# Optimization experiments

Hardware: AMD Instinct MI355X
Metric: run time of the kernel (lower is better)

The kernel has to match this reference:

```python
import jax, jax.numpy as jnp
import numpy as np

B_, L_, DM, DS, DC, EX = 4, 2048, 1024, 16, 4, 2
DI = DM * EX

def setup_inputs() -> dict:
    key = jax.random.key(0)
    ks = jax.random.split(key, 8)
    s = lambda i, shape, scale: jax.random.normal(ks[i], shape, jnp.float32) * scale
    return dict(
        x=s(0, (B_, L_, DM), 1.0),
        in_proj_w=s(1, (2 * DI, DM), 0.02),
        conv_weight=s(2, (DI, DC), 0.1),
        conv_bias=jnp.zeros((DI,), jnp.float32),
        A_log=jax.random.uniform(ks[3], (DS,), jnp.float32, -4.0, -1.0),
        D=jnp.ones((DI,), jnp.float32),
        delta_w=s(4, (DS, DI), 0.02),
        delta_b=jnp.ones((DS,), jnp.float32),
        B_w=s(5, (DS, DI), 0.02),
        C_w=s(6, (DS, DI), 0.02),
        out_proj_w=s(7, (DM, DI), 0.02),
    )

def reference(x, in_proj_w, conv_weight, conv_bias, A_log, D, delta_w, delta_b, B_w, C_w, out_proj_w):
    Bb, L, Dm = x.shape
    di, dc = conv_weight.shape
    # 1. input projection and split into ssm / gate branches
    x_inner = x @ in_proj_w.T                       # [B,L,2*di]
    x_ssm, x_gate = x_inner[..., :di], x_inner[..., di:]
    # 2. causal depthwise conv1d + SiLU (kernel size dc, per-channel weights)
    xp = jnp.pad(x_ssm, ((0, 0), (dc - 1, 0), (0, 0)))
    xc = conv_bias + sum(xp[:, k:k + L, :] * conv_weight[:, k] for k in range(dc))
    x_conv = jax.nn.silu(xc)                         # [B,L,di]
    # 3. content-aware discretization
    delta = jax.nn.softplus(x_conv @ delta_w.T + delta_b)  # [B,L,N]
    Bs = x_conv @ B_w.T                              # [B,L,N]
    Cs = x_conv @ C_w.T                              # [B,L,N]
    A = -jnp.exp(A_log)                              # [N]
    xavg = x_conv.mean(axis=-1)                      # [B,L]
    # 4. selective SSM scan over L with state h:[B,N]
    def step(h, inp):
        dt, bt, ct, xa = inp                         # [B,N],[B,N],[B,N],[B]
        h = jnp.exp(dt * A) * h + dt * bt * xa[:, None]
        return h, (h * ct).sum(-1)                   # y_t: [B]
    h0 = jnp.zeros((Bb, A.shape[0]), x.dtype)
    _, ys = jax.lax.scan(
        step, h0,
        (delta.transpose(1, 0, 2), Bs.transpose(1, 0, 2), Cs.transpose(1, 0, 2), xavg.T))
    y_ssm = ys.T[..., None]                          # [B,L,1] (broadcasts over di)
    # 5. gate, skip, output projection
    y_gated = y_ssm * jax.nn.silu(x_gate)
    y_skip = y_gated + x_conv * D
    return y_skip @ out_proj_w.T                     # [B,L,D]
```

## Files before the change

kernel.cpp:

```cpp
#include <hip/hip_runtime.h>
#include <cmath>

#define LL 2048
#define NROW 8192
#define DMODEL 1024
#define DINNER 2048
#define NSTATE 16
#define NSEG 64
#define SEGLEN 32

typedef unsigned short u16;
typedef __attribute__((ext_vector_type(8))) unsigned short u16x8;
typedef __attribute__((ext_vector_type(8))) short short8;
typedef __attribute__((ext_vector_type(4))) float floatx4;
typedef __attribute__((ext_vector_type(16))) float floatx16;

__device__ __forceinline__ float bf2f(u16 h) {
    unsigned u = ((unsigned)h) << 16;
    float f;
    __builtin_memcpy(&f, &u, 4);
    return f;
}
__device__ __forceinline__ u16 f2bf(float f) {
    unsigned u;
    __builtin_memcpy(&u, &f, 4);
    u = u + 0x7fffu + ((u >> 16) & 1u);
    return (u16)(u >> 16);
}
__device__ __forceinline__ float silu_f(float x) { return x / (1.f + __expf(-x)); }

__global__ __launch_bounds__(256) void cvt_multi(
    const float* __restrict__ s0, const float* __restrict__ s1,
    const float* __restrict__ s2, const float* __restrict__ s3,
    const float* __restrict__ s4, const float* __restrict__ s5,
    u16* __restrict__ d0, u16* __restrict__ d1, u16* __restrict__ d2,
    u16* __restrict__ d3, u16* __restrict__ d4, u16* __restrict__ d5) {
    int bid = blockIdx.x;
    const float* s;
    u16* d;
    size_t off;
    if (bid < 4096)      { s = s0; d = d0; off = (size_t)bid * 2048; }
    else if (bid < 6144) { s = s1; d = d1; off = (size_t)(bid - 4096) * 2048; }
    else if (bid < 7168) { s = s2; d = d2; off = (size_t)(bid - 6144) * 2048; }
    else if (bid < 7184) { s = s3; d = d3; off = (size_t)(bid - 7168) * 2048; }
    else if (bid < 7200) { s = s4; d = d4; off = (size_t)(bid - 7184) * 2048; }
    else                 { s = s5; d = d5; off = (size_t)(bid - 7200) * 2048; }
    size_t i = off + (size_t)threadIdx.x * 8;
    float4 a = *(const float4*)&s[i];
    float4 b = *(const float4*)&s[i + 4];
    u16x8 o;
    o[0] = f2bf(a.x); o[1] = f2bf(a.y); o[2] = f2bf(a.z); o[3] = f2bf(a.w);
    o[4] = f2bf(b.x); o[5] = f2bf(b.y); o[6] = f2bf(b.z); o[7] = f2bf(b.w);
    *(u16x8*)&d[i] = o;
}

#define GL_LDS(gp, lp)                                                        \
    __builtin_amdgcn_global_load_lds(                                         \
        (const __attribute__((address_space(1))) void*)(gp),                  \
        (__attribute__((address_space(3))) void*)(lp), 16, 0, 0)
#define BAR() __builtin_amdgcn_s_barrier()
#define SB0() __builtin_amdgcn_sched_barrier(0)
#define LGKM0()                                                               \
    do {                                                                      \
        asm volatile("s_waitcnt lgkmcnt(0)" ::: "memory");                    \
        __builtin_amdgcn_sched_barrier(0);                                    \
    } while (0)
#define VMC4() asm volatile("s_waitcnt vmcnt(4)" ::: "memory")
#define VMC2() asm volatile("s_waitcnt vmcnt(2)" ::: "memory")
#define PRIO1() __builtin_amdgcn_s_setprio(1)
#define PRIO0() __builtin_amdgcn_s_setprio(0)

template <int OUT_BF16>
__global__ __launch_bounds__(512, 2) void gemm_bt_256(
    const u16* __restrict__ A, const u16* __restrict__ B,
    void* __restrict__ Cout, int N, int K) {
    __shared__ u16 sAf[2 * 2 * 128 * 64];
    __shared__ u16 sBf[2 * 2 * 128 * 64];
    const int tid = threadIdx.x;
    const int lane = tid & 63;
    const int wave = tid >> 6;
    const int wm = wave >> 2;
    const int wn = wave & 3;

    const int gx = gridDim.x;
    const int nwg = gx * gridDim.y;
    const int cpx = nwg >> 3;
    int lin = blockIdx.y * gx + blockIdx.x;
    int swz = (lin & 7) * cpx + (lin >> 3);
    const int bm = (swz / gx) * 256;
    const int bn = (swz % gx) * 256;

    const int gslot = (lane & 7) ^ ((lane >> 3) & 7);
    const int srowoff = lane >> 3;
    const u16* aStage = A + (size_t)(bm + wave * 8 + srowoff) * K + gslot * 8 + 64;
    const u16* bStage = B + (size_t)(bn + wave * 8 + srowoff) * K + gslot * 8 + 128;
    const size_t row64 = (size_t)64 * K;
    const size_t row128 = (size_t)128 * K;

#define STAGE_A(BUF, H, PTR)                                                  \
    do {                                                                      \
        GL_LDS((PTR) + (H) * row128,         &sAf[(BUF) * 16384 + (H) * 8192 + wave * 512]); \
        GL_LDS((PTR) + (H) * row128 + row64, &sAf[(BUF) * 16384 + (H) * 8192 + (8 + wave) * 512]); \
    } while (0)
#define STAGE_B(BUF, H, PTR)                                                  \
    do {                                                                      \
        GL_LDS((PTR) + (H) * row128,         &sBf[(BUF) * 16384 + (H) * 8192 + wave * 512]); \
        GL_LDS((PTR) + (H) * row128 + row64, &sBf[(BUF) * 16384 + (H) * 8192 + (8 + wave) * 512]); \
    } while (0)

    const int fr = lane & 15;
    const int kq = lane >> 4;
    const int st0 = kq ^ (fr & 7);
    const int st1 = (4 + kq) ^ (fr & 7);
    const int aRd0 = wm * 8192 + fr * 64 + st0 * 8;
    const int aRd1 = wm * 8192 + fr * 64 + st1 * 8;
    const int bRow = (wn & 1) * 64 + fr;
    const int bRd0 = (wn >> 1) * 8192 + bRow * 64 + st0 * 8;
    const int bRd1 = (wn >> 1) * 8192 + bRow * 64 + st1 * 8;

#define RD_A(dst, BUF, R0)                                                    \
    do {                                                                      \
        _Pragma("unroll")                                                     \
        for (int mi = 0; mi < 4; ++mi) {                                      \
            dst[mi][0] = *(const short8*)&sAf[(BUF) * 16384 + aRd0 + ((R0) + mi * 16) * 64]; \
            dst[mi][1] = *(const short8*)&sAf[(BUF) * 16384 + aRd1 + ((R0) + mi * 16) * 64]; \
        }                                                                     \
    } while (0)
#define RD_B(dst, BUF, R0)                                                    \
    do {                                                                      \
        _Pragma("unroll")                                                     \
        for (int ni = 0; ni < 2; ++ni) {                                      \
            dst[ni][0] = *(const short8*)&sBf[(BUF) * 16384 + bRd0 + ((R0) + ni * 16) * 64]; \
            dst[ni][1] = *(const short8*)&sBf[(BUF) * 16384 + bRd1 + ((R0) + ni * 16) * 64]; \
        }                                                                     \
    } while (0)
#define MFMA_PH(AF, RB, BF, CB)                                               \
    do {                                                                      \
        _Pragma("unroll")                                                     \
        for (int kh = 0; kh < 2; ++kh)                                        \
            _Pragma("unroll")                                                 \
            for (int mi = 0; mi < 4; ++mi)                                    \
                _Pragma("unroll")                                             \
                for (int ni = 0; ni < 2; ++ni)                                \
                    acc[(RB) + mi][(CB) + ni] =                               \
                        __builtin_amdgcn_mfma_f32_16x16x32_bf16(              \
                            AF[mi][kh], BF[ni][kh],                           \
                            acc[(RB) + mi][(CB) + ni], 0, 0, 0);              \
    } while (0)

    floatx4 acc[8][4];
#pragma unroll
    for (int i = 0; i < 8; ++i)
#pragma unroll
        for (int j = 0; j < 4; ++j) acc[i][j] = (floatx4){0.f, 0.f, 0.f, 0.f};

    short8 afX[4][2], afY[4][2], bf01[2][2], bf23[2][2];

    {
        const u16* a0 = aStage - 64;
        const u16* b0 = bStage - 128;
        STAGE_A(0, 0, a0);
        STAGE_A(0, 1, a0);
        STAGE_B(0, 0, b0);
        STAGE_B(0, 1, b0);
        STAGE_B(1, 0, b0 + 64);
        STAGE_B(1, 1, b0 + 64);
    }
    VMC4();
    BAR();
    RD_A(afX, 0, 0);
    RD_B(bf01, 0, 0);
    SB0();

#define TILE(CUR, NXT)                                                        \
                      \
    LGKM0();                                                                  \
    PRIO1();                                                                  \
    MFMA_PH(afX, 0, bf01, 0);                                                 \
    PRIO0();                                                                  \
    SB0();                                                                    \
    RD_B(bf23, CUR, 32);                                                      \
    STAGE_A(NXT, 0, aStage);                                                  \
    SB0();                                                                    \
             \
    LGKM0();                                                                  \
    PRIO1();                                                                  \
    MFMA_PH(afX, 0, bf23, 2);                                                 \
    PRIO0();                                                                  \
    SB0();                                                                    \
    RD_A(afY, CUR, 64);                                                       \
    STAGE_A(NXT, 1, aStage);                                                  \
    VMC4();                                                \
    BAR();                                                                    \
                     \
    LGKM0();                                                                  \
    PRIO1();                                                                  \
    MFMA_PH(afY, 4, bf01, 0);                                                 \
    PRIO0();                                                                  \
    SB0();                                                                    \
    RD_B(bf01, NXT, 0);                                                       \
    STAGE_B(CUR, 0, bStage);                                                  \
    SB0();                                                                    \
            \
    PRIO1();                                                                  \
    MFMA_PH(afY, 4, bf23, 2);                                                 \
    PRIO0();                                                                  \
    SB0();                                                                    \
    STAGE_B(CUR, 1, bStage);                                                  \
    VMC4();                                                \
    BAR();                                                                    \
    RD_A(afX, NXT, 0);                                                        \
    SB0();                                                                    \
    aStage += 64;                                                             \
    bStage += 64;

    const int NT = K >> 6;
    for (int t = 0; t < NT; t += 2) {
        TILE(0, 1)
        TILE(1, 0)
    }
#undef TILE

    const int cc = lane & 15;
    const int rb = (lane >> 4) * 4;
#pragma unroll
    for (int mi = 0; mi < 8; ++mi)
#pragma unroll
        for (int ni = 0; ni < 4; ++ni)
#pragma unroll
            for (int r = 0; r < 4; ++r) {
                int grow = bm + wm * 128 + mi * 16 + rb + r;
                int gcol = bn + wn * 64 + ni * 16 + cc;
                float v = acc[mi][ni][r];
                if (OUT_BF16)
                    ((u16*)Cout)[(size_t)grow * N + gcol] = f2bf(v);
                else
                    ((float*)Cout)[(size_t)grow * N + gcol] = v;
            }
#undef STAGE_A
#undef STAGE_B
#undef RD_A
#undef RD_B
#undef MFMA_PH
}

template <int OUT_BF16>
__global__ __launch_bounds__(512, 4) void gemm_bt_128p(
    const u16* __restrict__ A, const u16* __restrict__ B,
    void* __restrict__ Cout, int N, int K) {
    __shared__ u16 sAf[2 * 128 * 64];
    __shared__ u16 sBf[2 * 128 * 64];
    const int tid = threadIdx.x;
    const int lane = tid & 63;
    const int wave = tid >> 6;
    const int wm = wave >> 2;
    const int wn = wave & 3;

    const int gx = gridDim.x;
    const int nwg = gx * gridDim.y;
    const int cpx = nwg >> 3;
    int lin = blockIdx.y * gx + blockIdx.x;
    int swz = (lin & 7) * cpx + (lin >> 3);
    const int bm = (swz / gx) * 128;
    const int bn = (swz % gx) * 128;

    const int gslot = (lane & 7) ^ ((lane >> 3) & 7);
    const int srowoff = lane >> 3;
    const u16* aStage = A + (size_t)(bm + wave * 8 + srowoff) * K + gslot * 8 + 64;
    const u16* bStage = B + (size_t)(bn + wave * 8 + srowoff) * K + gslot * 8 + 128;
    const size_t row64 = (size_t)64 * K;

#define STAGE_A(BUF, PTR)                                                     \
    do {                                                                      \
        GL_LDS((PTR),         &sAf[(BUF) * 8192 + wave * 512]);               \
        GL_LDS((PTR) + row64, &sAf[(BUF) * 8192 + (8 + wave) * 512]);         \
    } while (0)
#define STAGE_B(BUF, PTR)                                                     \
    do {                                                                      \
        GL_LDS((PTR),         &sBf[(BUF) * 8192 + wave * 512]);               \
        GL_LDS((PTR) + row64, &sBf[(BUF) * 8192 + (8 + wave) * 512]);         \
    } while (0)

    const int fr = lane & 15;
    const int kq = lane >> 4;
    const int st0 = kq ^ (fr & 7);
    const int st1 = (4 + kq) ^ (fr & 7);
    const int aRd0 = (wm * 64 + fr) * 64 + st0 * 8;
    const int aRd1 = (wm * 64 + fr) * 64 + st1 * 8;
    const int bRd0 = (wn * 32 + fr) * 64 + st0 * 8;
    const int bRd1 = (wn * 32 + fr) * 64 + st1 * 8;

#define RD_A(dst, BUF)                                                        \
    do {                                                                      \
        _Pragma("unroll")                                                     \
        for (int mi = 0; mi < 4; ++mi) {                                      \
            dst[mi][0] = *(const short8*)&sAf[(BUF) * 8192 + aRd0 + mi * 16 * 64]; \
            dst[mi][1] = *(const short8*)&sAf[(BUF) * 8192 + aRd1 + mi * 16 * 64]; \
        }                                                                     \
    } while (0)
#define RD_B(dst, BUF, NI)                                                    \
    do {                                                                      \
        dst[0] = *(const short8*)&sBf[(BUF) * 8192 + bRd0 + (NI) * 16 * 64];  \
        dst[1] = *(const short8*)&sBf[(BUF) * 8192 + bRd1 + (NI) * 16 * 64];  \
    } while (0)
#define MFMA8(BF, NI)                                                         \
    do {                                                                      \
        _Pragma("unroll")                                                     \
        for (int kh = 0; kh < 2; ++kh)                                        \
            _Pragma("unroll")                                                 \
            for (int mi = 0; mi < 4; ++mi)                                    \
                acc[mi][NI] = __builtin_amdgcn_mfma_f32_16x16x32_bf16(        \
                    afc[mi][kh], BF[kh], acc[mi][NI], 0, 0, 0);               \
    } while (0)

    floatx4 acc[4][2];
#pragma unroll
    for (int i = 0; i < 4; ++i)
#pragma unroll
        for (int j = 0; j < 2; ++j) acc[i][j] = (floatx4){0.f, 0.f, 0.f, 0.f};

    short8 afc[4][2], bf0[2], bf1[2];

    STAGE_A(0, aStage - 64);
    STAGE_B(0, bStage - 128);
    STAGE_B(1, bStage - 64);
    VMC2();
    BAR();
    RD_A(afc, 0);
    RD_B(bf0, 0, 0);
    SB0();

#define TILE(CUR, NXT)                                                        \
                              \
    LGKM0();                                                                  \
    PRIO1();                                                                  \
    MFMA8(bf0, 0);                                                            \
    PRIO0();                                                                  \
    SB0();                                                                    \
    RD_B(bf1, CUR, 1);                                                        \
    STAGE_A(NXT, aStage);                                                     \
    BAR();                                                                    \
                  \
    LGKM0();                                                                  \
    PRIO1();                                                                  \
    MFMA8(bf1, 1);                                                            \
    PRIO0();                                                                  \
    SB0();                                                                    \
    STAGE_B(CUR, bStage);                                                     \
    VMC2();                      \
    BAR();                                                                    \
    RD_A(afc, NXT);                                                           \
    RD_B(bf0, NXT, 0);                                                        \
    SB0();                                                                    \
    aStage += 64;                                                             \
    bStage += 64;

    const int NT = K >> 6;
    for (int t = 0; t < NT; t += 2) {
        TILE(0, 1)
        TILE(1, 0)
    }
#undef TILE

    asm volatile("s_waitcnt vmcnt(0)" ::: "memory");

    const int cc = lane & 15;
    const int rb = (lane >> 4) * 4;
#pragma unroll
    for (int mi = 0; mi < 4; ++mi)
#pragma unroll
        for (int ni = 0; ni < 2; ++ni)
#pragma unroll
            for (int r = 0; r < 4; ++r) {
                int grow = bm + wm * 64 + mi * 16 + rb + r;
                int gcol = bn + wn * 32 + ni * 16 + cc;
                float v = acc[mi][ni][r];
                if (OUT_BF16)
                    ((u16*)Cout)[(size_t)grow * N + gcol] = f2bf(v);
                else
                    ((float*)Cout)[(size_t)grow * N + gcol] = v;
            }
#undef STAGE_A
#undef STAGE_B
#undef RD_A
#undef RD_B
#undef MFMA8
}

__global__ __launch_bounds__(256) void conv_silu_avg(
    const u16* __restrict__ xin, const float* __restrict__ cw,
    const float* __restrict__ cb, u16* __restrict__ xconv,
    float* __restrict__ xavg) {
    const int blk = blockIdx.x;
    const int b = blk >> 7;
    const int lc = blk & 127;
    const int row0 = b * LL + lc * 16;
    const int tid = threadIdx.x;
    const int lane = tid & 63, wave = tid >> 6;
    const int d0 = tid * 8;
    float4 cwv[8];
    float cbv[8];
#pragma unroll
    for (int e = 0; e < 8; ++e) cwv[e] = *(const float4*)&cw[(d0 + e) * 4];
#pragma unroll
    for (int e = 0; e < 8; e += 4) {
        float4 c = *(const float4*)&cb[d0 + e];
        cbv[e] = c.x; cbv[e + 1] = c.y; cbv[e + 2] = c.z; cbv[e + 3] = c.w;
    }
    u16x8 w0, w1, w2;
    if (lc == 0) {
        w0 = (u16x8)0; w1 = (u16x8)0; w2 = (u16x8)0;
    } else {
        w0 = *(const u16x8*)&xin[(size_t)(row0 - 3) * (2 * DINNER) + d0];
        w1 = *(const u16x8*)&xin[(size_t)(row0 - 2) * (2 * DINNER) + d0];
        w2 = *(const u16x8*)&xin[(size_t)(row0 - 1) * (2 * DINNER) + d0];
    }
    float sums[16];
#pragma unroll
    for (int t = 0; t < 16; ++t) {
        u16x8 cur = *(const u16x8*)&xin[(size_t)(row0 + t) * (2 * DINNER) + d0];
        float lsum = 0.f;
        u16x8 o;
#pragma unroll
        for (int e = 0; e < 8; ++e) {
            float acc = cbv[e];
            acc += bf2f(w0[e]) * cwv[e].x;
            acc += bf2f(w1[e]) * cwv[e].y;
            acc += bf2f(w2[e]) * cwv[e].z;
            acc += bf2f(cur[e]) * cwv[e].w;
            float s = silu_f(acc);
            lsum += s;
            o[e] = f2bf(s);
        }
        *(u16x8*)&xconv[(size_t)(row0 + t) * DINNER + d0] = o;
        sums[t] = lsum;
        w0 = w1; w1 = w2; w2 = cur;
    }
#pragma unroll
    for (int off = 32; off; off >>= 1)
#pragma unroll
        for (int t = 0; t < 16; ++t) sums[t] += __shfl_down(sums[t], off);
    __shared__ float wred[4][16];
    if (lane == 0) {
#pragma unroll
        for (int t = 0; t < 16; ++t) wred[wave][t] = sums[t];
    }
    __syncthreads();
    if (tid < 16)
        xavg[row0 + tid] = (wred[0][tid] + wred[1][tid] + wred[2][tid] + wred[3][tid]) *
                           (1.f / DINNER);
}

__global__ __launch_bounds__(256) void dbc_direct(
    const u16* __restrict__ xconv, const u16* __restrict__ wcat,
    const float* __restrict__ db, const float* __restrict__ A_log,
    const float* __restrict__ xavg,
    float* __restrict__ a_out, float* __restrict__ u_out, float* __restrict__ c_out) {
    __shared__ float part[4][32][48];
    const int tid = threadIdx.x;
    const int lane = tid & 63;
    const int wave = tid >> 6;
    const int bm = blockIdx.x * 32;
    const int fr = lane & 15;
    const int kq = lane >> 4;
    const int k0 = wave * 512 + kq * 8;

    const u16* ap0 = xconv + (size_t)(bm + fr) * DINNER + k0;
    const u16* ap1 = xconv + (size_t)(bm + 16 + fr) * DINNER + k0;
    const u16* bp0 = wcat + (size_t)(fr) * DINNER + k0;
    const u16* bp1 = wcat + (size_t)(16 + fr) * DINNER + k0;
    const u16* bp2 = wcat + (size_t)(32 + fr) * DINNER + k0;

    floatx4 acc[2][3];
#pragma unroll
    for (int mi = 0; mi < 2; ++mi)
#pragma unroll
        for (int ni = 0; ni < 3; ++ni) acc[mi][ni] = (floatx4){0.f, 0.f, 0.f, 0.f};

#pragma unroll 4
    for (int kk = 0; kk < 16; ++kk) {
        short8 a0 = *(const short8*)ap0;
        short8 a1 = *(const short8*)ap1;
        short8 b0 = *(const short8*)bp0;
        short8 b1 = *(const short8*)bp1;
        short8 b2 = *(const short8*)bp2;
        ap0 += 32; ap1 += 32; bp0 += 32; bp1 += 32; bp2 += 32;
        acc[0][0] = __builtin_amdgcn_mfma_f32_16x16x32_bf16(a0, b0, acc[0][0], 0, 0, 0);
        acc[0][1] = __builtin_amdgcn_mfma_f32_16x16x32_bf16(a0, b1, acc[0][1], 0, 0, 0);
        acc[0][2] = __builtin_amdgcn_mfma_f32_16x16x32_bf16(a0, b2, acc[0][2], 0, 0, 0);
        acc[1][0] = __builtin_amdgcn_mfma_f32_16x16x32_bf16(a1, b0, acc[1][0], 0, 0, 0);
        acc[1][1] = __builtin_amdgcn_mfma_f32_16x16x32_bf16(a1, b1, acc[1][1], 0, 0, 0);
        acc[1][2] = __builtin_amdgcn_mfma_f32_16x16x32_bf16(a1, b2, acc[1][2], 0, 0, 0);
    }
    const int cr = kq * 4;
#pragma unroll
    for (int mi = 0; mi < 2; ++mi)
#pragma unroll
        for (int ni = 0; ni < 3; ++ni)
#pragma unroll
            for (int r = 0; r < 4; ++r)
                part[wave][mi * 16 + cr + r][ni * 16 + fr] = acc[mi][ni][r];
    __syncthreads();
#pragma unroll
    for (int it = tid; it < 512; it += 256) {
        int row = it >> 4;
        int s = it & 15;
        float sd = 0.f, sb = 0.f, sc = 0.f;
#pragma unroll
        for (int w = 0; w < 4; ++w) {
            sd += part[w][row][s];
            sb += part[w][row][s + 16];
            sc += part[w][row][s + 32];
        }
        int grow = bm + row;
        float Aa = -__expf(A_log[s]);
        float pre = sd + db[s];
        float delta = (pre > 20.f) ? pre : log1pf(__expf(pre));
        a_out[grow * NSTATE + s] = __expf(delta * Aa);
        u_out[grow * NSTATE + s] = delta * sb * xavg[grow];
        c_out[grow * NSTATE + s] = sc;
    }
}

__global__ __launch_bounds__(1024) void scan_fused(
    const float* __restrict__ a, const float* __restrict__ u,
    const float* __restrict__ c, float* __restrict__ y) {
    const int b = blockIdx.x;
    const int tid = threadIdx.x;
    const int s = tid & 15;
    const int seg = tid >> 4;
    __shared__ float Ps[NSEG][NSTATE];
    __shared__ float Hs[NSEG][NSTATE];
    __shared__ float HSs[NSEG][NSTATE];

    size_t base = (size_t)(b * LL + seg * SEGLEN) * NSTATE + s;
    float P = 1.f, h = 0.f;
#pragma unroll 8
    for (int t = 0; t < SEGLEN; ++t) {
        float av = a[base + (size_t)t * NSTATE];
        float uv = u[base + (size_t)t * NSTATE];
        h = fmaf(av, h, uv);
        P *= av;
    }
    Ps[seg][s] = P;
    Hs[seg][s] = h;
    __syncthreads();
    if (tid < 16) {
        float hh = 0.f;
        for (int g = 0; g < NSEG; ++g) {
            HSs[g][tid] = hh;
            hh = fmaf(Ps[g][tid], hh, Hs[g][tid]);
        }
    }
    __syncthreads();
    float h2 = HSs[seg][s];
#pragma unroll 8
    for (int t = 0; t < SEGLEN; ++t) {
        float av = a[base + (size_t)t * NSTATE];
        float uv = u[base + (size_t)t * NSTATE];
        float cv = c[base + (size_t)t * NSTATE];
        h2 = fmaf(av, h2, uv);
        float p = h2 * cv;
        p += __shfl_xor(p, 1);
        p += __shfl_xor(p, 2);
        p += __shfl_xor(p, 4);
        p += __shfl_xor(p, 8);
        if (s == 0) y[b * LL + seg * SEGLEN + t] = p;
    }
}

__global__ __launch_bounds__(256) void gate_skip(
    const u16* __restrict__ xin, const float* __restrict__ y,
    const float* __restrict__ Dv, const u16* __restrict__ xconv,
    u16* __restrict__ yskip) {
    size_t i = ((size_t)blockIdx.x * 256 + threadIdx.x) * 8;
    int row = (int)(i >> 11);
    int d = (int)(i & (DINNER - 1));
    u16x8 g = *(const u16x8*)&xin[(size_t)row * (2 * DINNER) + DINNER + d];
    u16x8 xc = *(const u16x8*)&xconv[i];
    float yv = y[row];
    u16x8 o;
#pragma unroll
    for (int e = 0; e < 8; ++e) {
        float gv = silu_f(bf2f(g[e]));
        float v = yv * gv + bf2f(xc[e]) * Dv[d + e];
        o[e] = f2bf(v);
    }
    *(u16x8*)&yskip[i] = o;
}

extern "C" void kernel_launch(void* const* d_in, const int* in_sizes, int n_in,
                              void* d_out, int out_size, void* d_ws, size_t ws_size,
                              hipStream_t stream) {
    const float* x       = (const float*)d_in[0];
    const float* w_in    = (const float*)d_in[1];
    const float* conv_w  = (const float*)d_in[2];
    const float* conv_b  = (const float*)d_in[3];
    const float* A_log   = (const float*)d_in[4];
    const float* Dv      = (const float*)d_in[5];
    const float* delta_w = (const float*)d_in[6];
    const float* delta_b = (const float*)d_in[7];
    const float* B_w     = (const float*)d_in[8];
    const float* C_w     = (const float*)d_in[9];
    const float* out_w   = (const float*)d_in[10];
    float* out = (float*)d_out;

    u16* xb  = (u16*)d_ws;
    u16* wb  = xb + 8388608;
    u16* owb = wb + 4194304;
    u16* wsb = owb + 2097152;
    u16* xin = wsb + 98304;
    u16* xcv = xin + 33554432;
    u16* ysk = xcv + 16777216;
    float* fb     = (float*)(ysk + 16777216);
    float* abuf   = fb;
    float* ubuf   = abuf + 131072;
    float* cbuf   = ubuf + 131072;
    float* ybuf   = cbuf + 131072;
    float* avgbuf = ybuf + 8192;

    cvt_multi<<<7216, 256, 0, stream>>>(x, w_in, out_w, delta_w, B_w, C_w,
                                        xb, wb, owb, wsb, wsb + 32768, wsb + 65536);

    gemm_bt_256<1><<<dim3(16, 32), 512, 0, stream>>>(xb, wb, xin, 2 * DINNER, DMODEL);

    conv_silu_avg<<<512, 256, 0, stream>>>(xin, conv_w, conv_b, xcv, avgbuf);
    dbc_direct<<<256, 256, 0, stream>>>(xcv, wsb, delta_b, A_log, avgbuf,
                                        abuf, ubuf, cbuf);

    scan_fused<<<4, 1024, 0, stream>>>(abuf, ubuf, cbuf, ybuf);

    gate_skip<<<NROW * DINNER / 8 / 256, 256, 0, stream>>>(xin, ybuf, Dv, xcv, ysk);

    gemm_bt_128p<0><<<dim3(8, 64), 512, 0, stream>>>(ysk, owb, out, DMODEL, DINNER);
}
```

Before: 288.5 us.

## Fuse conv+SiLU+mean kernel with delta/B/C projection via LDS tile

Merges the depthwise conv/SiLU/row-mean kernel with the small delta/B/C projection kernel. Each block keeps its 16 conv output rows in an LDS tile (padded stride) and runs the MFMA projection straight from LDS, so x_conv is no longer re-read from global memory and one launch plus the xavg round trip go away. The cost is about 66KB of LDS per block, which limits occupancy, and half-size M tiles for the MFMA work, so the weight matrix is re-read by twice as many blocks.

Measured after the change: 295.2 us. +2.3%, slower.

```diff
diff --git a/kernel.cpp b/kernel.cpp
--- a/kernel.cpp
+++ b/kernel.cpp
@@ -201,7 +201,7 @@
     RD_B(bf01, NXT, 0);                                                       \
     STAGE_B(CUR, 0, bStage);                                                  \
     SB0();                                                                    \
-            \
+                 \
     PRIO1();                                                                  \
     MFMA_PH(afY, 4, bf23, 2);                                                 \
     PRIO0();                                                                  \
@@ -331,7 +331,6 @@
     SB0();
 
 #define TILE(CUR, NXT)                                                        \
-                              \
     LGKM0();                                                                  \
     PRIO1();                                                                  \
     MFMA8(bf0, 0);                                                            \
@@ -340,7 +339,6 @@
     RD_B(bf1, CUR, 1);                                                        \
     STAGE_A(NXT, aStage);                                                     \
     BAR();                                                                    \
-                  \
     LGKM0();                                                                  \
     PRIO1();                                                                  \
     MFMA8(bf1, 1);                                                            \
@@ -387,10 +385,18 @@
 #undef MFMA8
 }
 
-__global__ __launch_bounds__(256) void conv_silu_avg(
+#define XT_STRIDE 2056
+__global__ __launch_bounds__(256) void conv_dbc(
     const u16* __restrict__ xin, const float* __restrict__ cw,
-    const float* __restrict__ cb, u16* __restrict__ xconv,
-    float* __restrict__ xavg) {
+    const float* __restrict__ cb, const u16* __restrict__ wcat,
+    const float* __restrict__ db, const float* __restrict__ A_log,
+    u16* __restrict__ xconv,
+    float* __restrict__ a_out, float* __restrict__ u_out,
+    float* __restrict__ c_out) {
+    __shared__ u16 xtile[16 * XT_STRIDE];
+    __shared__ float part[4][16][48];
+    __shared__ float wred[4][16];
+    __shared__ float xa[16];
     const int blk = blockIdx.x;
     const int b = blk >> 7;
     const int lc = blk & 127;
@@ -398,6 +404,7 @@
     const int tid = threadIdx.x;
     const int lane = tid & 63, wave = tid >> 6;
     const int d0 = tid * 8;
+
     float4 cwv[8];
     float cbv[8];
 #pragma unroll
@@ -433,6 +440,7 @@
             o[e] = f2bf(s);
         }
         *(u16x8*)&xconv[(size_t)(row0 + t) * DINNER + d0] = o;
+        *(u16x8*)&xtile[t * XT_STRIDE + d0] = o;
         sums[t] = lsum;
         w0 = w1; w1 = w2; w2 = cur;
     }
@@ -440,84 +448,60 @@
     for (int off = 32; off; off >>= 1)
 #pragma unroll
         for (int t = 0; t < 16; ++t) sums[t] += __shfl_down(sums[t], off);
-    __shared__ float wred[4][16];
     if (lane == 0) {
 #pragma unroll
         for (int t = 0; t < 16; ++t) wred[wave][t] = sums[t];
     }
     __syncthreads();
     if (tid < 16)
-        xavg[row0 + tid] = (wred[0][tid] + wred[1][tid] + wred[2][tid] + wred[3][tid]) *
-                           (1.f / DINNER);
-}
-
-__global__ __launch_bounds__(256) void dbc_direct(
-    const u16* __restrict__ xconv, const u16* __restrict__ wcat,
-    const float* __restrict__ db, const float* __restrict__ A_log,
-    const float* __restrict__ xavg,
-    float* __restrict__ a_out, float* __restrict__ u_out, float* __restrict__ c_out) {
-    __shared__ float part[4][32][48];
-    const int tid = threadIdx.x;
-    const int lane = tid & 63;
-    const int wave = tid >> 6;
-    const int bm = blockIdx.x * 32;
+        xa[tid] = (wred[0][tid] + wred[1][tid] + wred[2][tid] + wred[3][tid]) *
+                  (1.f / DINNER);
+    __syncthreads();
+
     const int fr = lane & 15;
     const int kq = lane >> 4;
     const int k0 = wave * 512 + kq * 8;
-
-    const u16* ap0 = xconv + (size_t)(bm + fr) * DINNER + k0;
-    const u16* ap1 = xconv + (size_t)(bm + 16 + fr) * DINNER + k0;
-    const u16* bp0 = wcat + (size_t)(fr) * DINNER + k0;
+    const u16* bp0 = wcat + (size_t)fr * DINNER + k0;
     const u16* bp1 = wcat + (size_t)(16 + fr) * DINNER + k0;
     const u16* bp2 = wcat + (size_t)(32 + fr) * DINNER + k0;
-
-    floatx4 acc[2][3];
-#pragma unroll
-    for (int mi = 0; mi < 2; ++mi)
-#pragma unroll
-        for (int ni = 0; ni < 3; ++ni) acc[mi][ni] = (floatx4){0.f, 0.f, 0.f, 0.f};
+    const int aBase = fr * XT_STRIDE + k0;
+
+    floatx4 pacc[3];
+#pragma unroll
+    for (int ni = 0; ni < 3; ++ni) pacc[ni] = (floatx4){0.f, 0.f, 0.f, 0.f};
 
 #pragma unroll 4
     for (int kk = 0; kk < 16; ++kk) {
-        short8 a0 = *(const short8*)ap0;
-        short8 a1 = *(const short8*)ap1;
-        short8 b0 = *(const short8*)bp0;
-        short8 b1 = *(const short8*)bp1;
-        short8 b2 = *(const short8*)bp2;
-        ap0 += 32; ap1 += 32; bp0 += 32; bp1 += 32; bp2 += 32;
-        acc[0][0] = __builtin_amdgcn_mfma_f32_16x16x32_bf16(a0, b0, acc[0][0], 0, 0, 0);
-        acc[0][1] = __builtin_amdgcn_mfma_f32_16x16x32_bf16(a0, b1, acc[0][1], 0, 0, 0);
-        acc[0][2] = __builtin_amdgcn_mfma_f32_16x16x32_bf16(a0, b2, acc[0][2], 0, 0, 0);
-        acc[1][0] = __builtin_amdgcn_mfma_f32_16x16x32_bf16(a1, b0, acc[1][0], 0, 0, 0);
-        acc[1][1] = __builtin_amdgcn_mfma_f32_16x16x32_bf16(a1, b1, acc[1][1], 0, 0, 0);
-        acc[1][2] = __builtin_amdgcn_mfma_f32_16x16x32_bf16(a1, b2, acc[1][2], 0, 0, 0);
+        short8 a0 = *(const short8*)&xtile[aBase + kk * 32];
+        short8 b0 = *(const short8*)(bp0 + kk * 32);
+        short8 b1 = *(const short8*)(bp1 + kk * 32);
+        short8 b2 = *(const short8*)(bp2 + kk * 32);
+        pacc[0] = __builtin_amdgcn_mfma_f32_16x16x32_bf16(a0, b0, pacc[0], 0, 0, 0);
+        pacc[1] = __builtin_amdgcn_mfma_f32_16x16x32_bf16(a0, b1, pacc[1], 0, 0, 0);
+        pacc[2] = __builtin_amdgcn_mfma_f32_16x16x32_bf16(a0, b2, pacc[2], 0, 0, 0);
     }
     const int cr = kq * 4;
 #pragma unroll
-    for (int mi = 0; mi < 2; ++mi)
-#pragma unroll
-        for (int ni = 0; ni < 3; ++ni)
-#pragma unroll
-            for (int r = 0; r < 4; ++r)
-                part[wave][mi * 16 + cr + r][ni * 16 + fr] = acc[mi][ni][r];
+    for (int ni = 0; ni < 3; ++ni)
+#pragma unroll
+        for (int r = 0; r < 4; ++r)
+            part[wave][cr + r][ni * 16 + fr] = pacc[ni][r];
     __syncthreads();
-#pragma unroll
-    for (int it = tid; it < 512; it += 256) {
-        int row = it >> 4;
-        int s = it & 15;
-        float sd = 0.f, sb = 0.f, sc = 0.f;
-#pragma unroll
-        for (int w = 0; w < 4; ++w) {
-            sd += part[w][row][s];
-            sb += part[w][row][s + 16];
-            sc += part[w][row][s + 32];
-        }
-        int grow = bm + row;
+
+    {
+        int row = tid >> 4;
+        int s = tid & 15;
+        float sd = part[0][row][s] + part[1][row][s] + part[2][row][s] + part[3][row][s];
+        float sb = part[0][row][s + 16] + part[1][row][s + 16] +
+                   part[2][row][s + 16] + part[3][row][s + 16];
+        float sc = part[0][row][s + 32] + part[1][row][s + 32] +
+                   part[2][row][s + 32] + part[3][row][s + 32];
+        int grow = row0 + row;
         float Aa = -__expf(A_log[s]);
         float pre = sd + db[s];
         float delta = (pre > 20.f) ? pre : log1pf(__expf(pre));
         a_out[grow * NSTATE + s] = __expf(delta * Aa);
-        u_out[grow * NSTATE + s] = delta * sb * xavg[grow];
+        u_out[grow * NSTATE + s] = delta * sb * xa[row];
         c_out[grow * NSTATE + s] = sc;
     }
 }
@@ -617,16 +601,14 @@
     float* ubuf   = abuf + 131072;
     float* cbuf   = ubuf + 131072;
     float* ybuf   = cbuf + 131072;
-    float* avgbuf = ybuf + 8192;
 
     cvt_multi<<<7216, 256, 0, stream>>>(x, w_in, out_w, delta_w, B_w, C_w,
                                         xb, wb, owb, wsb, wsb + 32768, wsb + 65536);
 
     gemm_bt_256<1><<<dim3(16, 32), 512, 0, stream>>>(xb, wb, xin, 2 * DINNER, DMODEL);
 
-    conv_silu_avg<<<512, 256, 0, stream>>>(xin, conv_w, conv_b, xcv, avgbuf);
-    dbc_direct<<<256, 256, 0, stream>>>(xcv, wsb, delta_b, A_log, avgbuf,
-                                        abuf, ubuf, cbuf);
+    conv_dbc<<<512, 256, 0, stream>>>(xin, conv_w, conv_b, wsb, delta_b, A_log,
+                                      xcv, abuf, ubuf, cbuf);
 
     scan_fused<<<4, 1024, 0, stream>>>(abuf, ubuf, cbuf, ybuf);
 
```
